# Optimization experiments

Measured on AMD Instinct MI355X. Metric: run time of the kernel, lower is better.

The kernel has to match this reference:

```python
import jax, jax.numpy as jnp
import numpy as np

N_NODES = 50000


def setup_inputs() -> dict:
    key = jax.random.key(0)
    k1, k2, k3, k4 = jax.random.split(key, 4)
    in_c, hid = 256, 128
    x = jax.random.normal(k1, (N_NODES, in_c), dtype=jnp.float32)
    edge_index = jax.random.randint(k2, (2, 800000), 0, N_NODES, dtype=jnp.int32)
    # GCNConv weight (glorot) and bias
    W_conv = jax.random.normal(k3, (in_c, hid), dtype=jnp.float32) * (1.0 / np.sqrt(in_c))
    b_conv = jnp.zeros((hid,), dtype=jnp.float32)
    # Final Linear (xavier_uniform per reset_parameters)
    limit = np.sqrt(6.0 / (hid + in_c))
    W_lin = jax.random.uniform(k4, (hid, in_c), dtype=jnp.float32, minval=-limit, maxval=limit)
    b_lin = jnp.zeros((in_c,), dtype=jnp.float32)
    return {"x": x, "edge_index": edge_index, "W_conv": W_conv, "b_conv": b_conv,
            "W_lin": W_lin, "b_lin": b_lin}


def _gcn_conv(x, edge_index, W, b):
    n = x.shape[0]
    # add self-loops (standard GCN normalization)
    loop = jnp.arange(n, dtype=edge_index.dtype)
    src = jnp.concatenate([edge_index[0], loop])
    dst = jnp.concatenate([edge_index[1], loop])
    # transform first (in_c -> hid) so the edge gather moves the smaller dim
    h = x @ W  # [N, hid]
    deg = jax.ops.segment_sum(jnp.ones_like(dst, dtype=h.dtype), dst, num_segments=n)
    dinv = jnp.where(deg > 0, jax.lax.rsqrt(deg), 0.0)
    norm = dinv[src] * dinv[dst]  # [E+N]
    msg = h[src] * norm[:, None]  # [E+N, hid]
    out = jax.ops.segment_sum(msg, dst, num_segments=n)
    return out + b


def reference(x, edge_index, W_conv, b_conv, W_lin, b_lin):
    h = _gcn_conv(x, edge_index, W_conv, b_conv)  # [N, hid]
    # dropout p=0.0 -> identity
    return h @ W_lin + b_lin  # [N, in_c]
```

## Files before the change

### kernel.cpp

```cpp
#include <hip/hip_runtime.h>
#include <hip/hip_fp16.h>


#define N_NODES 50000
#define N_EDGES 800000
#define IN_C 256
#define HID 128
#define SCAN_BLOCKS ((N_NODES + 255) / 256)
#define GEMM_MBLK ((N_NODES + 63) / 64)
#define PREP_BLOCKS 1024
#define BUCKET_BLOCKS 2048
#define LDK 72

#define OFF_H    0UL
#define OFF_CONV 12800000UL
#define OFF_DEG  25600000UL
#define OFF_RP   25800000UL
#define OFF_DINV 26000064UL
#define OFF_RANK 26200064UL
#define OFF_REC  27800064UL
#define OFF_BSUM 31000064UL
#define OFF_WT1  31001088UL
#define OFF_WT2  31066624UL

typedef __attribute__((ext_vector_type(8))) short bf16x8;
typedef __attribute__((ext_vector_type(4))) float f32x4;

__device__ __forceinline__ ushort f2bf(float x) {
    unsigned u = __float_as_uint(x);
    u += 0x7fffu + ((u >> 16) & 1u);
    return (ushort)(u >> 16);
}

__global__ __launch_bounds__(256) void prep_kernel(
    const float* __restrict__ Wc, const float* __restrict__ Wl,
    ushort* __restrict__ wtc, ushort* __restrict__ wtl,
    const int* __restrict__ dst, ushort* __restrict__ rank, int* __restrict__ deg)
{
    int i = blockIdx.x * 256 + threadIdx.x;
    if (i < HID * IN_C) {
        int n = i / IN_C, k = i % IN_C;
        wtc[i] = f2bf(Wc[k * HID + n]);
    } else if (i < 2 * HID * IN_C) {
        int j = i - HID * IN_C;
        int n = j / HID, k = j % HID;
        wtl[j] = f2bf(Wl[k * IN_C + n]);
    }
    for (int e = i; e < N_EDGES; e += PREP_BLOCKS * 256)
        rank[e] = (ushort)atomicAdd(&deg[dst[e]], 1);
}

__global__ __launch_bounds__(256) void scan_blocks_kernel(
    const int* __restrict__ deg, int* __restrict__ row_ptr,
    int* __restrict__ bsums, int n)
{
    __shared__ int tmp[256];
    int tid = threadIdx.x;
    int i = blockIdx.x * 256 + tid;
    int v = (i < n) ? deg[i] : 0;
    int orig = v;
    tmp[tid] = v;
    __syncthreads();
    #pragma unroll
    for (int off = 1; off < 256; off <<= 1) {
        int t = (tid >= off) ? tmp[tid - off] : 0;
        __syncthreads();
        tmp[tid] += t;
        __syncthreads();
    }
    if (i < n) row_ptr[i] = tmp[tid] - orig;
    if (tid == 255) bsums[blockIdx.x] = tmp[255];
}

__global__ __launch_bounds__(256) void finalize2_kernel(
    const int* __restrict__ deg, int* __restrict__ row_ptr,
    const int* __restrict__ bsums, float* __restrict__ dinv, int n)
{
    __shared__ int tmp[256];
    __shared__ int orig[256];
    int tid = threadIdx.x;
    int v = (tid < SCAN_BLOCKS) ? bsums[tid] : 0;
    tmp[tid] = v;
    orig[tid] = v;
    __syncthreads();
    #pragma unroll
    for (int off = 1; off < 256; off <<= 1) {
        int t = (tid >= off) ? tmp[tid - off] : 0;
        __syncthreads();
        tmp[tid] += t;
        __syncthreads();
    }
    int boff = tmp[blockIdx.x] - orig[blockIdx.x];
    int i = blockIdx.x * 256 + tid;
    if (i < n) {
        row_ptr[i] += boff;
        dinv[i] = rsqrtf((float)(deg[i] + 1));
    }
    if (i == 0) row_ptr[n] = N_EDGES;
}

__global__ __launch_bounds__(256) void bucket_kernel(
    const int* __restrict__ src, const int* __restrict__ dst,
    const ushort* __restrict__ rank, const int* __restrict__ row_ptr,
    const float* __restrict__ dinv, unsigned* __restrict__ rec)
{
    int cls = blockIdx.x & 7;
    int blk = blockIdx.x >> 3;
    int lo = cls * (N_NODES / 8);
    int hi = lo + (N_NODES / 8);
    const int CHUNK = (N_EDGES + 255) / 256;
    int e0 = blk * CHUNK;
    int e1 = min(e0 + CHUNK, N_EDGES);
    for (int i = e0 + threadIdx.x; i < e1; i += 256) {
        int d = dst[i];
        if (d >= lo && d < hi) {
            int s = src[i];
            unsigned r = (unsigned)(ushort)s |
                         ((unsigned)__half_as_ushort(__float2half_rn(dinv[s])) << 16);
            rec[row_ptr[d] + rank[i]] = r;
        }
    }
}

template <int KT, bool A_IS_BF16, bool BF16OUT>
__global__ __launch_bounds__(256) void mfma_gemm_kernel(
    const void* __restrict__ Av, const ushort* __restrict__ Bt,
    const float* __restrict__ bias, void* __restrict__ Cv,
    int M, int N)
{
    constexpr int NIT = KT / 64;
    __shared__ __align__(16) ushort As[64 * LDK];
    __shared__ __align__(16) ushort Bs[128 * LDK];
    int tid = threadIdx.x;
    int wave = tid >> 6, lane = tid & 63;
    int quad = lane >> 4, l16 = lane & 15;
    int wm0 = (wave >> 1) * 32, wn0 = (wave & 1) * 64;
    int bm = blockIdx.x * 64, bn = blockIdx.y * 128;

    int arow = tid >> 2, acol = (tid & 3) * 16;
    int agrow = bm + arow;
    int brow = tid >> 1, bkk = (tid & 1) * 32;

    f32x4 acc[2][4] = {};
    float4 a32[2][4];
    bf16x8 a16[2][2];
    bf16x8 breg[2][4];

    auto issue = [&](int it, int s) {
        int k0 = it * 64;
        if (A_IS_BF16) {
            a16[s][0] = bf16x8{};
            a16[s][1] = bf16x8{};
            if (agrow < M) {
                const ushort* ap = (const ushort*)Av + (size_t)agrow * KT + k0 + acol;
                a16[s][0] = *(const bf16x8*)ap;
                a16[s][1] = *(const bf16x8*)(ap + 8);
            }
        } else {
            a32[s][0] = a32[s][1] = a32[s][2] = a32[s][3] = make_float4(0.f, 0.f, 0.f, 0.f);
            if (agrow < M) {
                const float* ap = (const float*)Av + (size_t)agrow * KT + k0 + acol;
                a32[s][0] = *(const float4*)ap;
                a32[s][1] = *(const float4*)(ap + 4);
                a32[s][2] = *(const float4*)(ap + 8);
                a32[s][3] = *(const float4*)(ap + 12);
            }
        }
        const ushort* bp = Bt + (size_t)(bn + brow) * KT + k0 + bkk;
        breg[s][0] = *(const bf16x8*)bp;
        breg[s][1] = *(const bf16x8*)(bp + 8);
        breg[s][2] = *(const bf16x8*)(bp + 16);
        breg[s][3] = *(const bf16x8*)(bp + 24);
    };

    auto stage = [&](int s) {
        if (A_IS_BF16) {
            *(bf16x8*)&As[arow * LDK + acol]     = a16[s][0];
            *(bf16x8*)&As[arow * LDK + acol + 8] = a16[s][1];
        } else {
            ushort t0[8] = {f2bf(a32[s][0].x), f2bf(a32[s][0].y), f2bf(a32[s][0].z), f2bf(a32[s][0].w),
                            f2bf(a32[s][1].x), f2bf(a32[s][1].y), f2bf(a32[s][1].z), f2bf(a32[s][1].w)};
            ushort t1[8] = {f2bf(a32[s][2].x), f2bf(a32[s][2].y), f2bf(a32[s][2].z), f2bf(a32[s][2].w),
                            f2bf(a32[s][3].x), f2bf(a32[s][3].y), f2bf(a32[s][3].z), f2bf(a32[s][3].w)};
            *(bf16x8*)&As[arow * LDK + acol]     = *(bf16x8*)t0;
            *(bf16x8*)&As[arow * LDK + acol + 8] = *(bf16x8*)t1;
        }
        *(bf16x8*)&Bs[brow * LDK + bkk]      = breg[s][0];
        *(bf16x8*)&Bs[brow * LDK + bkk + 8]  = breg[s][1];
        *(bf16x8*)&Bs[brow * LDK + bkk + 16] = breg[s][2];
        *(bf16x8*)&Bs[brow * LDK + bkk + 24] = breg[s][3];
    };

    issue(0, 0);
    #pragma unroll
    for (int it = 0; it < NIT; ++it) {
        int cur = it & 1;
        if (it + 1 < NIT) issue(it + 1, cur ^ 1);
        if (it > 0) __syncthreads();
        stage(cur);
        __syncthreads();
        bf16x8 af[2][2], bfr[4][2];
        #pragma unroll
        for (int im = 0; im < 2; ++im)
            #pragma unroll
            for (int kh = 0; kh < 2; ++kh)
                af[im][kh] = *(bf16x8*)&As[(wm0 + im * 16 + l16) * LDK + kh * 32 + quad * 8];
        #pragma unroll
        for (int in = 0; in < 4; ++in)
            #pragma unroll
            for (int kh = 0; kh < 2; ++kh)
                bfr[in][kh] = *(bf16x8*)&Bs[(wn0 + in * 16 + l16) * LDK + kh * 32 + quad * 8];
        #pragma unroll
        for (int im = 0; im < 2; ++im)
            #pragma unroll
            for (int in = 0; in < 4; ++in) {
                acc[im][in] = __builtin_amdgcn_mfma_f32_16x16x32_bf16(
                    af[im][0], bfr[in][0], acc[im][in], 0, 0, 0);
                acc[im][in] = __builtin_amdgcn_mfma_f32_16x16x32_bf16(
                    af[im][1], bfr[in][1], acc[im][in], 0, 0, 0);
            }
    }
    #pragma unroll
    for (int im = 0; im < 2; ++im) {
        #pragma unroll
        for (int in = 0; in < 4; ++in) {
            int col = bn + wn0 + in * 16 + l16;
            float bval = bias ? bias[col] : 0.f;
            #pragma unroll
            for (int r = 0; r < 4; ++r) {
                int grow = bm + wm0 + im * 16 + quad * 4 + r;
                if (grow < M) {
                    float o = acc[im][in][r] + bval;
                    if (BF16OUT)
                        ((ushort*)Cv)[(size_t)grow * N + col] = f2bf(o);
                    else
                        ((float*)Cv)[(size_t)grow * N + col] = o;
                }
            }
        }
    }
}

__device__ __forceinline__ void acc_edge(float4& acc, unsigned r,
                                         const ushort* __restrict__ hb, int c) {
    unsigned s = r & 0xffffu;
    float w = __half2float(__ushort_as_half((ushort)(r >> 16)));
    uint2 v = *(const uint2*)&hb[(size_t)s * HID + c];
    acc.x += w * __uint_as_float(v.x << 16);
    acc.y += w * __uint_as_float(v.x & 0xffff0000u);
    acc.z += w * __uint_as_float(v.y << 16);
    acc.w += w * __uint_as_float(v.y & 0xffff0000u);
}

__global__ __launch_bounds__(256) void gather_kernel(
    const ushort* __restrict__ hb, const int* __restrict__ row_ptr,
    const unsigned* __restrict__ rec, const float* __restrict__ dinv,
    const float* __restrict__ b_conv, ushort* __restrict__ convb, int n)
{
    int wave = threadIdx.x >> 6;
    int lane = threadIdx.x & 63;
    int d = blockIdx.x * 4 + wave;
    if (d >= n) return;
    int half = lane >> 5;
    int l32 = lane & 31;
    int c = l32 << 2;

    float4 acc = make_float4(0.f, 0.f, 0.f, 0.f);
    int begin = row_ptr[d], end = row_ptr[d + 1];
    int e = begin + half;
    for (; e + 6 < end; e += 8) {
        unsigned r0 = rec[e];
        unsigned r1 = rec[e + 2];
        unsigned r2 = rec[e + 4];
        unsigned r3 = rec[e + 6];
        acc_edge(acc, r0, hb, c);
        acc_edge(acc, r1, hb, c);
        acc_edge(acc, r2, hb, c);
        acc_edge(acc, r3, hb, c);
    }
    for (; e < end; e += 2) {
        unsigned r0 = rec[e];
        acc_edge(acc, r0, hb, c);
    }
    acc.x += __shfl_xor(acc.x, 32);
    acc.y += __shfl_xor(acc.y, 32);
    acc.z += __shfl_xor(acc.z, 32);
    acc.w += __shfl_xor(acc.w, 32);

    if (half == 0) {
        float di = dinv[d];
        uint2 hv = *(const uint2*)&hb[(size_t)d * HID + c];
        acc.x += di * __uint_as_float(hv.x << 16);
        acc.y += di * __uint_as_float(hv.x & 0xffff0000u);
        acc.z += di * __uint_as_float(hv.y << 16);
        acc.w += di * __uint_as_float(hv.y & 0xffff0000u);
        float4 bb = *(const float4*)&b_conv[c];
        float ox = di * acc.x + bb.x;
        float oy = di * acc.y + bb.y;
        float oz = di * acc.z + bb.z;
        float ow = di * acc.w + bb.w;
        uint2 po;
        po.x = ((unsigned)f2bf(oy) << 16) | (unsigned)f2bf(ox);
        po.y = ((unsigned)f2bf(ow) << 16) | (unsigned)f2bf(oz);
        *(uint2*)&convb[(size_t)d * HID + c] = po;
    }
}

extern "C" void kernel_launch(void* const* d_in, const int* in_sizes, int n_in,
                              void* d_out, int out_size, void* d_ws, size_t ws_size,
                              hipStream_t stream) {
    const float* x      = (const float*)d_in[0];
    const int*   ei     = (const int*)d_in[1];
    const float* W_conv = (const float*)d_in[2];
    const float* b_conv = (const float*)d_in[3];
    const float* W_lin  = (const float*)d_in[4];
    const float* b_lin  = (const float*)d_in[5];
    float* out = (float*)d_out;

    char* ws = (char*)d_ws;
    ushort* hb      = (ushort*)(ws + OFF_H);
    ushort* convb   = (ushort*)(ws + OFF_CONV);
    int*    deg     = (int*)(ws + OFF_DEG);
    int*    row_ptr = (int*)(ws + OFF_RP);
    float*  dinv    = (float*)(ws + OFF_DINV);
    ushort* rank    = (ushort*)(ws + OFF_RANK);
    unsigned* rec   = (unsigned*)(ws + OFF_REC);
    int*    bsums   = (int*)(ws + OFF_BSUM);
    ushort* wt_conv = (ushort*)(ws + OFF_WT1);
    ushort* wt_lin  = (ushort*)(ws + OFF_WT2);

    const int* src = ei;
    const int* dst = ei + N_EDGES;

    hipMemsetAsync(deg, 0, 200000, stream);

    prep_kernel<<<PREP_BLOCKS, 256, 0, stream>>>(W_conv, W_lin, wt_conv, wt_lin,
                                                 dst, rank, deg);
    scan_blocks_kernel<<<SCAN_BLOCKS, 256, 0, stream>>>(deg, row_ptr, bsums, N_NODES);
    finalize2_kernel<<<SCAN_BLOCKS, 256, 0, stream>>>(deg, row_ptr, bsums, dinv, N_NODES);

    bucket_kernel<<<BUCKET_BLOCKS, 256, 0, stream>>>(src, dst, rank, row_ptr, dinv, rec);

    mfma_gemm_kernel<IN_C, false, true><<<dim3(GEMM_MBLK, HID / 128), 256, 0, stream>>>(
        x, wt_conv, nullptr, hb, N_NODES, HID);

    gather_kernel<<<(N_NODES + 3) / 4, 256, 0, stream>>>(
        hb, row_ptr, rec, dinv, b_conv, convb, N_NODES);

    mfma_gemm_kernel<HID, true, false><<<dim3(GEMM_MBLK, IN_C / 128), 256, 0, stream>>>(
        convb, wt_lin, b_lin, out, N_NODES, IN_C);
}
```

Measured before the change: 231.9 us.

## Fuse CSR build and first GEMM into persistent kernel with grid barriers

Replaces the memset, degree-count, two scan kernels, bucket kernel and first GEMM with one persistent mega kernel of 512 blocks. Some blocks run the x@W GEMM tiles while the others do the degree atomics, then software grid barriers sequence the scan, finalize and bucket phases. This cuts launch overhead and overlaps edge counting with the GEMM. The cost is that only 384 blocks run the GEMM, and the spin barriers need every block co-resident, so the grid can deadlock if occupancy is too low.

```diff
diff --git a/kernel.cpp b/kernel.cpp
--- a/kernel.cpp
+++ b/kernel.cpp
@@ -8,8 +8,8 @@
 #define HID 128
 #define SCAN_BLOCKS ((N_NODES + 255) / 256)
 #define GEMM_MBLK ((N_NODES + 63) / 64)
-#define PREP_BLOCKS 1024
-#define BUCKET_BLOCKS 2048
+#define MEGA_BLOCKS 512
+#define GEMM1_BLOCKS 384
 #define LDK 72
 
 #define OFF_H    0UL
@@ -32,110 +32,48 @@
     return (ushort)(u >> 16);
 }
 
+__device__ __forceinline__ void gbar(int* bar, int target) {
+    __threadfence();
+    __syncthreads();
+    if (threadIdx.x == 0) {
+        __hip_atomic_fetch_add(bar, 1, __ATOMIC_ACQ_REL, __HIP_MEMORY_SCOPE_AGENT);
+        while (__hip_atomic_load(bar, __ATOMIC_ACQUIRE, __HIP_MEMORY_SCOPE_AGENT) < target)
+            __builtin_amdgcn_s_sleep(2);
+    }
+    __syncthreads();
+    __threadfence();
+}
+
 __global__ __launch_bounds__(256) void prep_kernel(
     const float* __restrict__ Wc, const float* __restrict__ Wl,
     ushort* __restrict__ wtc, ushort* __restrict__ wtl,
-    const int* __restrict__ dst, ushort* __restrict__ rank, int* __restrict__ deg)
+    int* __restrict__ deg, int* __restrict__ bar)
 {
     int i = blockIdx.x * 256 + threadIdx.x;
     if (i < HID * IN_C) {
         int n = i / IN_C, k = i % IN_C;
         wtc[i] = f2bf(Wc[k * HID + n]);
-    } else if (i < 2 * HID * IN_C) {
+    } else {
         int j = i - HID * IN_C;
         int n = j / HID, k = j % HID;
         wtl[j] = f2bf(Wl[k * IN_C + n]);
     }
-    for (int e = i; e < N_EDGES; e += PREP_BLOCKS * 256)
-        rank[e] = (ushort)atomicAdd(&deg[dst[e]], 1);
-}
-
-__global__ __launch_bounds__(256) void scan_blocks_kernel(
-    const int* __restrict__ deg, int* __restrict__ row_ptr,
-    int* __restrict__ bsums, int n)
-{
-    __shared__ int tmp[256];
-    int tid = threadIdx.x;
-    int i = blockIdx.x * 256 + tid;
-    int v = (i < n) ? deg[i] : 0;
-    int orig = v;
-    tmp[tid] = v;
-    __syncthreads();
-    #pragma unroll
-    for (int off = 1; off < 256; off <<= 1) {
-        int t = (tid >= off) ? tmp[tid - off] : 0;
-        __syncthreads();
-        tmp[tid] += t;
-        __syncthreads();
-    }
-    if (i < n) row_ptr[i] = tmp[tid] - orig;
-    if (tid == 255) bsums[blockIdx.x] = tmp[255];
-}
-
-__global__ __launch_bounds__(256) void finalize2_kernel(
-    const int* __restrict__ deg, int* __restrict__ row_ptr,
-    const int* __restrict__ bsums, float* __restrict__ dinv, int n)
-{
-    __shared__ int tmp[256];
-    __shared__ int orig[256];
-    int tid = threadIdx.x;
-    int v = (tid < SCAN_BLOCKS) ? bsums[tid] : 0;
-    tmp[tid] = v;
-    orig[tid] = v;
-    __syncthreads();
-    #pragma unroll
-    for (int off = 1; off < 256; off <<= 1) {
-        int t = (tid >= off) ? tmp[tid - off] : 0;
-        __syncthreads();
-        tmp[tid] += t;
-        __syncthreads();
-    }
-    int boff = tmp[blockIdx.x] - orig[blockIdx.x];
-    int i = blockIdx.x * 256 + tid;
-    if (i < n) {
-        row_ptr[i] += boff;
-        dinv[i] = rsqrtf((float)(deg[i] + 1));
-    }
-    if (i == 0) row_ptr[n] = N_EDGES;
-}
-
-__global__ __launch_bounds__(256) void bucket_kernel(
-    const int* __restrict__ src, const int* __restrict__ dst,
-    const ushort* __restrict__ rank, const int* __restrict__ row_ptr,
-    const float* __restrict__ dinv, unsigned* __restrict__ rec)
-{
-    int cls = blockIdx.x & 7;
-    int blk = blockIdx.x >> 3;
-    int lo = cls * (N_NODES / 8);
-    int hi = lo + (N_NODES / 8);
-    const int CHUNK = (N_EDGES + 255) / 256;
-    int e0 = blk * CHUNK;
-    int e1 = min(e0 + CHUNK, N_EDGES);
-    for (int i = e0 + threadIdx.x; i < e1; i += 256) {
-        int d = dst[i];
-        if (d >= lo && d < hi) {
-            int s = src[i];
-            unsigned r = (unsigned)(ushort)s |
-                         ((unsigned)__half_as_ushort(__float2half_rn(dinv[s])) << 16);
-            rec[row_ptr[d] + rank[i]] = r;
-        }
-    }
+    if (i < N_NODES) deg[i] = 0;
+    if (i == 0) *bar = 0;
 }
 
 template <int KT, bool A_IS_BF16, bool BF16OUT>
-__global__ __launch_bounds__(256) void mfma_gemm_kernel(
+__device__ __forceinline__ void gemm_tile_body(
     const void* __restrict__ Av, const ushort* __restrict__ Bt,
     const float* __restrict__ bias, void* __restrict__ Cv,
-    int M, int N)
+    int M, int N, int bx, int by, ushort* As, ushort* Bs)
 {
     constexpr int NIT = KT / 64;
-    __shared__ __align__(16) ushort As[64 * LDK];
-    __shared__ __align__(16) ushort Bs[128 * LDK];
     int tid = threadIdx.x;
     int wave = tid >> 6, lane = tid & 63;
     int quad = lane >> 4, l16 = lane & 15;
     int wm0 = (wave >> 1) * 32, wn0 = (wave & 1) * 64;
-    int bm = blockIdx.x * 64, bn = blockIdx.y * 128;
+    int bm = bx * 64, bn = by * 128;
 
     int arow = tid >> 2, acol = (tid & 3) * 16;
     int agrow = bm + arow;
@@ -220,6 +158,7 @@
                     af[im][1], bfr[in][1], acc[im][in], 0, 0, 0);
             }
     }
+    __syncthreads();
     #pragma unroll
     for (int im = 0; im < 2; ++im) {
         #pragma unroll
@@ -236,6 +175,104 @@
                     else
                         ((float*)Cv)[(size_t)grow * N + col] = o;
                 }
+            }
+        }
+    }
+}
+
+template <int KT, bool A_IS_BF16, bool BF16OUT>
+__global__ __launch_bounds__(256) void mfma_gemm_kernel(
+    const void* __restrict__ Av, const ushort* __restrict__ Bt,
+    const float* __restrict__ bias, void* __restrict__ Cv, int M, int N)
+{
+    __shared__ __align__(16) ushort As[64 * LDK];
+    __shared__ __align__(16) ushort Bs[128 * LDK];
+    gemm_tile_body<KT, A_IS_BF16, BF16OUT>(Av, Bt, bias, Cv, M, N,
+                                           blockIdx.x, blockIdx.y, As, Bs);
+}
+
+__global__ __launch_bounds__(256, 2) void mega_kernel(
+    const float* __restrict__ x, const ushort* __restrict__ wt_conv,
+    ushort* __restrict__ hb,
+    const int* __restrict__ src, const int* __restrict__ dst,
+    ushort* __restrict__ rank, int* __restrict__ deg,
+    int* __restrict__ row_ptr, int* __restrict__ bsums,
+    float* __restrict__ dinv, unsigned* __restrict__ rec, int* __restrict__ bar)
+{
+    __shared__ __align__(16) ushort smem[64 * LDK + 128 * LDK];
+    int bid = blockIdx.x;
+    int tid = threadIdx.x;
+
+    if (bid < GEMM1_BLOCKS) {
+        for (int t = bid; t < GEMM_MBLK; t += GEMM1_BLOCKS)
+            gemm_tile_body<IN_C, false, true>(x, wt_conv, nullptr, hb,
+                                              N_NODES, HID, t, 0,
+                                              smem, smem + 64 * LDK);
+    } else {
+        const int nb = MEGA_BLOCKS - GEMM1_BLOCKS;
+        for (int e = (bid - GEMM1_BLOCKS) * 256 + tid; e < N_EDGES; e += nb * 256)
+            rank[e] = (ushort)atomicAdd(&deg[dst[e]], 1);
+    }
+    gbar(bar, MEGA_BLOCKS);
+
+    if (bid < SCAN_BLOCKS) {
+        int* tmp = (int*)smem;
+        int i = bid * 256 + tid;
+        int v = (i < N_NODES) ? deg[i] : 0;
+        int orig = v;
+        tmp[tid] = v;
+        __syncthreads();
+        #pragma unroll
+        for (int off = 1; off < 256; off <<= 1) {
+            int t = (tid >= off) ? tmp[tid - off] : 0;
+            __syncthreads();
+            tmp[tid] += t;
+            __syncthreads();
+        }
+        if (i < N_NODES) row_ptr[i] = tmp[tid] - orig;
+        if (tid == 255) bsums[bid] = tmp[255];
+    }
+    gbar(bar, 2 * MEGA_BLOCKS);
+
+    if (bid < SCAN_BLOCKS) {
+        int* tmp = (int*)smem;
+        int* orig = tmp + 256;
+        int v = (tid < SCAN_BLOCKS) ? bsums[tid] : 0;
+        tmp[tid] = v;
+        orig[tid] = v;
+        __syncthreads();
+        #pragma unroll
+        for (int off = 1; off < 256; off <<= 1) {
+            int t = (tid >= off) ? tmp[tid - off] : 0;
+            __syncthreads();
+            tmp[tid] += t;
+            __syncthreads();
+        }
+        int boff = tmp[bid] - orig[bid];
+        int i = bid * 256 + tid;
+        if (i < N_NODES) {
+            row_ptr[i] += boff;
+            dinv[i] = rsqrtf((float)(deg[i] + 1));
+        }
+        if (i == 0) row_ptr[N_NODES] = N_EDGES;
+    }
+    gbar(bar, 3 * MEGA_BLOCKS);
+
+    {
+        int cls = bid & 7;
+        int blk = bid >> 3;
+        int lo = cls * (N_NODES / 8);
+        int hi = lo + (N_NODES / 8);
+        const int CHUNK = (N_EDGES + 63) / 64;
+        int e0 = blk * CHUNK;
+        int e1 = min(e0 + CHUNK, N_EDGES);
+        for (int i = e0 + tid; i < e1; i += 256) {
+            int d = dst[i];
+            if (d >= lo && d < hi) {
+                int s = src[i];
+                unsigned r = (unsigned)(ushort)s |
+                             ((unsigned)__half_as_ushort(__float2half_rn(dinv[s])) << 16);
+                rec[row_ptr[d] + rank[i]] = r;
             }
         }
     }
@@ -328,21 +365,15 @@
     int*    bsums   = (int*)(ws + OFF_BSUM);
     ushort* wt_conv = (ushort*)(ws + OFF_WT1);
     ushort* wt_lin  = (ushort*)(ws + OFF_WT2);
+    int*    bar     = bsums + 255;
 
     const int* src = ei;
     const int* dst = ei + N_EDGES;
 
-    hipMemsetAsync(deg, 0, 200000, stream);
-
-    prep_kernel<<<PREP_BLOCKS, 256, 0, stream>>>(W_conv, W_lin, wt_conv, wt_lin,
-                                                 dst, rank, deg);
-    scan_blocks_kernel<<<SCAN_BLOCKS, 256, 0, stream>>>(deg, row_ptr, bsums, N_NODES);
-    finalize2_kernel<<<SCAN_BLOCKS, 256, 0, stream>>>(deg, row_ptr, bsums, dinv, N_NODES);
-
-    bucket_kernel<<<BUCKET_BLOCKS, 256, 0, stream>>>(src, dst, rank, row_ptr, dinv, rec);
-
-    mfma_gemm_kernel<IN_C, false, true><<<dim3(GEMM_MBLK, HID / 128), 256, 0, stream>>>(
-        x, wt_conv, nullptr, hb, N_NODES, HID);
+    prep_kernel<<<256, 256, 0, stream>>>(W_conv, W_lin, wt_conv, wt_lin, deg, bar);
+
+    mega_kernel<<<MEGA_BLOCKS, 256, 0, stream>>>(
+        x, wt_conv, hb, src, dst, rank, deg, row_ptr, bsums, dinv, rec, bar);
 
     gather_kernel<<<(N_NODES + 3) / 4, 256, 0, stream>>>(
         hb, row_ptr, rec, dinv, b_conv, convb, N_NODES);
```

Result: slower. 613.2 us (+164.5%).

## Fuse neighbor aggregation with final linear GEMM in one kernel

Applied to the files above, without the earlier changes.

The gather kernel and the second GEMM are merged. Each block aggregates 64 destination rows into an LDS tile in bf16, then multiplies that tile by W_lin with MFMA and writes the final output. This removes the round trip of the conv result through global memory and one launch. In exchange the gather runs with far fewer blocks (782 instead of 12500, 16 rows serially per wave), which lowers latency hiding for the irregular gathers.

```diff
diff --git a/kernel.cpp b/kernel.cpp
--- a/kernel.cpp
+++ b/kernel.cpp
@@ -11,6 +11,7 @@
 #define PREP_BLOCKS 1024
 #define BUCKET_BLOCKS 2048
 #define LDK 72
+#define LDK2 136
 
 #define OFF_H    0UL
 #define OFF_CONV 12800000UL
@@ -252,57 +253,124 @@
     acc.w += w * __uint_as_float(v.y & 0xffff0000u);
 }
 
-__global__ __launch_bounds__(256) void gather_kernel(
+__global__ __launch_bounds__(256) void gather_gemm2_kernel(
     const ushort* __restrict__ hb, const int* __restrict__ row_ptr,
     const unsigned* __restrict__ rec, const float* __restrict__ dinv,
-    const float* __restrict__ b_conv, ushort* __restrict__ convb, int n)
-{
-    int wave = threadIdx.x >> 6;
-    int lane = threadIdx.x & 63;
-    int d = blockIdx.x * 4 + wave;
-    if (d >= n) return;
+    const float* __restrict__ b_conv, const ushort* __restrict__ wt_lin,
+    const float* __restrict__ b_lin, float* __restrict__ out)
+{
+    __shared__ __align__(16) ushort As[64 * LDK2];
+    __shared__ __align__(16) ushort Bs[128 * LDK];
+    int tid = threadIdx.x;
+    int wave = tid >> 6, lane = tid & 63;
+    int bm = blockIdx.x * 64;
     int half = lane >> 5;
     int l32 = lane & 31;
     int c = l32 << 2;
 
-    float4 acc = make_float4(0.f, 0.f, 0.f, 0.f);
-    int begin = row_ptr[d], end = row_ptr[d + 1];
-    int e = begin + half;
-    for (; e + 6 < end; e += 8) {
-        unsigned r0 = rec[e];
-        unsigned r1 = rec[e + 2];
-        unsigned r2 = rec[e + 4];
-        unsigned r3 = rec[e + 6];
-        acc_edge(acc, r0, hb, c);
-        acc_edge(acc, r1, hb, c);
-        acc_edge(acc, r2, hb, c);
-        acc_edge(acc, r3, hb, c);
-    }
-    for (; e < end; e += 2) {
-        unsigned r0 = rec[e];
-        acc_edge(acc, r0, hb, c);
-    }
-    acc.x += __shfl_xor(acc.x, 32);
-    acc.y += __shfl_xor(acc.y, 32);
-    acc.z += __shfl_xor(acc.z, 32);
-    acc.w += __shfl_xor(acc.w, 32);
-
-    if (half == 0) {
-        float di = dinv[d];
-        uint2 hv = *(const uint2*)&hb[(size_t)d * HID + c];
-        acc.x += di * __uint_as_float(hv.x << 16);
-        acc.y += di * __uint_as_float(hv.x & 0xffff0000u);
-        acc.z += di * __uint_as_float(hv.y << 16);
-        acc.w += di * __uint_as_float(hv.y & 0xffff0000u);
-        float4 bb = *(const float4*)&b_conv[c];
-        float ox = di * acc.x + bb.x;
-        float oy = di * acc.y + bb.y;
-        float oz = di * acc.z + bb.z;
-        float ow = di * acc.w + bb.w;
-        uint2 po;
-        po.x = ((unsigned)f2bf(oy) << 16) | (unsigned)f2bf(ox);
-        po.y = ((unsigned)f2bf(ow) << 16) | (unsigned)f2bf(oz);
-        *(uint2*)&convb[(size_t)d * HID + c] = po;
+    for (int j = 0; j < 16; ++j) {
+        int r = wave * 16 + j;
+        int d = bm + r;
+        float4 acc = make_float4(0.f, 0.f, 0.f, 0.f);
+        if (d < N_NODES) {
+            int begin = row_ptr[d], end = row_ptr[d + 1];
+            int e = begin + half;
+            for (; e + 6 < end; e += 8) {
+                unsigned r0 = rec[e];
+                unsigned r1 = rec[e + 2];
+                unsigned r2 = rec[e + 4];
+                unsigned r3 = rec[e + 6];
+                acc_edge(acc, r0, hb, c);
+                acc_edge(acc, r1, hb, c);
+                acc_edge(acc, r2, hb, c);
+                acc_edge(acc, r3, hb, c);
+            }
+            for (; e < end; e += 2) {
+                unsigned r0 = rec[e];
+                acc_edge(acc, r0, hb, c);
+            }
+        }
+        acc.x += __shfl_xor(acc.x, 32);
+        acc.y += __shfl_xor(acc.y, 32);
+        acc.z += __shfl_xor(acc.z, 32);
+        acc.w += __shfl_xor(acc.w, 32);
+        if (half == 0) {
+            uint2 po = make_uint2(0u, 0u);
+            if (d < N_NODES) {
+                float di = dinv[d];
+                uint2 hv = *(const uint2*)&hb[(size_t)d * HID + c];
+                acc.x += di * __uint_as_float(hv.x << 16);
+                acc.y += di * __uint_as_float(hv.x & 0xffff0000u);
+                acc.z += di * __uint_as_float(hv.y << 16);
+                acc.w += di * __uint_as_float(hv.y & 0xffff0000u);
+                float4 bb = *(const float4*)&b_conv[c];
+                float ox = di * acc.x + bb.x;
+                float oy = di * acc.y + bb.y;
+                float oz = di * acc.z + bb.z;
+                float ow = di * acc.w + bb.w;
+                po.x = ((unsigned)f2bf(oy) << 16) | (unsigned)f2bf(ox);
+                po.y = ((unsigned)f2bf(ow) << 16) | (unsigned)f2bf(oz);
+            }
+            *(uint2*)&As[r * LDK2 + c] = po;
+        }
+    }
+    __syncthreads();
+
+    int quad = lane >> 4, l16 = lane & 15;
+    int wm0 = (wave >> 1) * 32, wn0 = (wave & 1) * 64;
+    int brow = tid >> 1, bkk = (tid & 1) * 32;
+
+    #pragma unroll
+    for (int h = 0; h < 2; ++h) {
+        int bn = h * 128;
+        f32x4 acc2[2][4] = {};
+        #pragma unroll
+        for (int kq = 0; kq < 2; ++kq) {
+            int k0 = kq * 64;
+            {
+                const ushort* bp = wt_lin + (size_t)(bn + brow) * HID + k0 + bkk;
+                *(bf16x8*)&Bs[brow * LDK + bkk]      = *(const bf16x8*)bp;
+                *(bf16x8*)&Bs[brow * LDK + bkk + 8]  = *(const bf16x8*)(bp + 8);
+                *(bf16x8*)&Bs[brow * LDK + bkk + 16] = *(const bf16x8*)(bp + 16);
+                *(bf16x8*)&Bs[brow * LDK + bkk + 24] = *(const bf16x8*)(bp + 24);
+            }
+            __syncthreads();
+            bf16x8 af[2][2], bfr[4][2];
+            #pragma unroll
+            for (int im = 0; im < 2; ++im)
+                #pragma unroll
+                for (int kh = 0; kh < 2; ++kh)
+                    af[im][kh] = *(bf16x8*)&As[(wm0 + im * 16 + l16) * LDK2 + k0 + kh * 32 + quad * 8];
+            #pragma unroll
+            for (int in = 0; in < 4; ++in)
+                #pragma unroll
+                for (int kh = 0; kh < 2; ++kh)
+                    bfr[in][kh] = *(bf16x8*)&Bs[(wn0 + in * 16 + l16) * LDK + kh * 32 + quad * 8];
+            #pragma unroll
+            for (int im = 0; im < 2; ++im)
+                #pragma unroll
+                for (int in = 0; in < 4; ++in) {
+                    acc2[im][in] = __builtin_amdgcn_mfma_f32_16x16x32_bf16(
+                        af[im][0], bfr[in][0], acc2[im][in], 0, 0, 0);
+                    acc2[im][in] = __builtin_amdgcn_mfma_f32_16x16x32_bf16(
+                        af[im][1], bfr[in][1], acc2[im][in], 0, 0, 0);
+                }
+            __syncthreads();
+        }
+        #pragma unroll
+        for (int im = 0; im < 2; ++im) {
+            #pragma unroll
+            for (int in = 0; in < 4; ++in) {
+                int col = bn + wn0 + in * 16 + l16;
+                float bval = b_lin[col];
+                #pragma unroll
+                for (int r = 0; r < 4; ++r) {
+                    int grow = bm + wm0 + im * 16 + quad * 4 + r;
+                    if (grow < N_NODES)
+                        out[(size_t)grow * IN_C + col] = acc2[im][in][r] + bval;
+                }
+            }
+        }
     }
 }
 
@@ -319,7 +387,6 @@
 
     char* ws = (char*)d_ws;
     ushort* hb      = (ushort*)(ws + OFF_H);
-    ushort* convb   = (ushort*)(ws + OFF_CONV);
     int*    deg     = (int*)(ws + OFF_DEG);
     int*    row_ptr = (int*)(ws + OFF_RP);
     float*  dinv    = (float*)(ws + OFF_DINV);
@@ -344,9 +411,6 @@
     mfma_gemm_kernel<IN_C, false, true><<<dim3(GEMM_MBLK, HID / 128), 256, 0, stream>>>(
         x, wt_conv, nullptr, hb, N_NODES, HID);
 
-    gather_kernel<<<(N_NODES + 3) / 4, 256, 0, stream>>>(
-        hb, row_ptr, rec, dinv, b_conv, convb, N_NODES);
-
-    mfma_gemm_kernel<HID, true, false><<<dim3(GEMM_MBLK, IN_C / 128), 256, 0, stream>>>(
-        convb, wt_lin, b_lin, out, N_NODES, IN_C);
-}
+    gather_gemm2_kernel<<<GEMM_MBLK, 256, 0, stream>>>(
+        hb, row_ptr, rec, dinv, b_conv, wt_lin, b_lin, out);
+}
```

After: 246.6 us. +6.4%, slower.
